# Performance work log

Measured on AMD Instinct MI355X. Metric: run time of the kernel, lower is better.

Reference implementation:

```python
import jax, jax.numpy as jnp
import numpy as np

B, N, M, D, H = 4, 2048, 2048, 1024, 16
HD = D // H


def setup_inputs() -> dict:
    key = jax.random.key(0)
    ks = jax.random.split(key, 16)
    s = 1.0 / np.sqrt(D)
    inp = {
        "Q": jax.random.normal(ks[0], (B, N, D), jnp.float32),
        "K": jax.random.normal(ks[1], (B, M, D), jnp.float32),
        "V": jax.random.normal(ks[2], (B, M, D), jnp.float32),
        "attn_bias": jax.random.normal(ks[3], (B, N, M), jnp.float32),
        "mask": jax.random.randint(ks[4], (B, M), 0, 2).astype(bool),
        # linear params (torch nn.Linear: y = x @ W.T + b)
        "Wq": jax.random.uniform(ks[5], (D, D), jnp.float32, -s, s),
        "bq": jax.random.uniform(ks[6], (D,), jnp.float32, -s, s),
        "Wk": jax.random.uniform(ks[7], (D, D), jnp.float32, -s, s),
        "bk": jax.random.uniform(ks[8], (D,), jnp.float32, -s, s),
        "Wv": jax.random.uniform(ks[9], (D, D), jnp.float32, -s, s),
        "bv": jax.random.uniform(ks[10], (D,), jnp.float32, -s, s),
        "Wo": jax.random.uniform(ks[11], (D, D), jnp.float32, -s, s),
        "bo": jax.random.uniform(ks[12], (D,), jnp.float32, -s, s),
    }
    return inp


def reference(Q, K, V, attn_bias, mask, Wq, bq, Wk, bk, Wv, bv, Wo, bo):
    b, n, d = Q.shape
    m = K.shape[1]
    # bias (B,N,M) -> (B,1,N,M); mask (B,M) True = masked out (-inf)
    bias = attn_bias[:, None, :, :]
    bias = jnp.where(mask[:, None, None, :], -jnp.inf, bias)
    # projections, split heads: (B, H, len, head_dim)
    q = (Q @ Wq.T + bq).reshape(b, n, H, HD).transpose(0, 2, 1, 3)
    k = (K @ Wk.T + bk).reshape(b, m, H, HD).transpose(0, 2, 1, 3)
    v = (V @ Wv.T + bv).reshape(b, m, H, HD).transpose(0, 2, 1, 3)
    scale = 1.0 / np.sqrt(HD).astype(np.float32)
    attn = jnp.einsum("bhid,bhjd->bhij", q * scale, k) + bias
    attn = jax.nn.softmax(attn, axis=-1)
    out = jnp.einsum("bhij,bhjd->bhid", attn, v)
    out = out.transpose(0, 2, 1, 3).reshape(b, n, d)
    return out @ Wo.T + bo
```

## Files before the change

kernel.cpp:

```cpp
#include <hip/hip_runtime.h>
#include <hip/hip_bf16.h>

#define Bq 4
#define Nq 2048
#define Mq 2048
#define Dq 1024
#define Hq 16

typedef __attribute__((ext_vector_type(8))) short short8;
typedef __attribute__((ext_vector_type(4))) short short4v;
typedef __attribute__((ext_vector_type(4))) float floatx4;
typedef __attribute__((ext_vector_type(16))) float floatx16;
typedef __attribute__((ext_vector_type(4))) unsigned uint4v;

static __device__ __forceinline__ short f2bf(float f) {
    __hip_bfloat16 h = __float2bfloat16(f);
    short r;
    __builtin_memcpy(&r, &h, 2);
    return r;
}
static __device__ __forceinline__ float bf2f(short s) {
    unsigned u = ((unsigned)(unsigned short)s) << 16;
    float f;
    __builtin_memcpy(&f, &u, 4);
    return f;
}
static __device__ __forceinline__ unsigned cvtpk_bf16(float lo, float hi) {
    unsigned r;
    asm("v_cvt_pk_bf16_f32 %0, %1, %2" : "=v"(r) : "v"(lo), "v"(hi));
    return r;
}
static __device__ __forceinline__ void swap32(unsigned &a, unsigned &b) {
    asm("v_permlane32_swap_b32 %0, %1" : "+v"(a), "+v"(b));
}
static __device__ __forceinline__ float exp2_fast(float x) {
    float r;
    asm("v_exp_f32 %0, %1" : "=v"(r) : "v"(x));
    return r;
}
static __device__ __forceinline__ void gld16(const void* g, void* l) {
    __builtin_amdgcn_global_load_lds(
        (const __attribute__((address_space(1))) unsigned int*)g,
        (__attribute__((address_space(3))) unsigned int*)l, 16, 0, 0);
}

__global__ void bias_prep(const float* __restrict__ bias, const int* __restrict__ mask,
                          short* __restrict__ out)
{
    const long i = ((long)blockIdx.x * 256 + threadIdx.x) * 8;
    const int m = (int)(i & (Mq - 1));
    const int b = (int)(i >> 22);
    floatx4 f0 = *(const floatx4*)(bias + i);
    floatx4 f1 = *(const floatx4*)(bias + i + 4);
    const int* mp = mask + b * Mq + m;
    short8 o;
#pragma unroll
    for (int e = 0; e < 4; ++e) {
        o[e]     = mp[e]     ? f2bf(-1e38f) : f2bf(f0[e] * 1.44269504f);
        o[e + 4] = mp[e + 4] ? f2bf(-1e38f) : f2bf(f1[e] * 1.44269504f);
    }
    *(short8*)(out + i) = o;
}

__global__ void cvt_bf(const float* __restrict__ s0, const float* __restrict__ s1,
                       const float* __restrict__ s2, const float* __restrict__ s3,
                       short* __restrict__ out, long per)
{
    const int z = blockIdx.y;
    const float* s = (z == 0) ? s0 : (z == 1) ? s1 : (z == 2) ? s2 : s3;
    short* d = out + (long)z * per;
    const long i = ((long)blockIdx.x * 256 + threadIdx.x) * 8;
    floatx4 f0 = *(const floatx4*)(s + i);
    floatx4 f1 = *(const floatx4*)(s + i + 4);
    short8 o;
#pragma unroll
    for (int e = 0; e < 4; ++e) { o[e] = f2bf(f0[e]); o[e + 4] = f2bf(f1[e]); }
    *(short8*)(d + i) = o;
}

struct GB {
    const short* A[3];
    const short* W[3];
    const float* bias[3];
    void* C[3];
    float scale[3];
    int omode[3];
};

__global__ __launch_bounds__(256, 3)
void gemm_all(GB gb, int K)
{
    __shared__ __align__(16) short As[2][128 * 32];
    __shared__ __align__(16) short Bs[2][128 * 32];

    const int z = blockIdx.z;
    const short* Ap = gb.A[z];
    const short* Wp = gb.W[z];

    const int tid = threadIdx.x;
    const int lane = tid & 63;
    const int wid = tid >> 6;
    const int wr = wid >> 1, wc = wid & 1;
    const int g = lane >> 4, c = lane & 15;
    const long row0 = (long)blockIdx.x * 128;
    const int col0 = blockIdx.y * 128;

    const int R0 = tid >> 2;
    const int ub = (tid & 3) ^ ((R0 >> 1) & 3);
    const short* asrc = Ap + (row0 + R0) * (long)K + ub * 8;
    const short* bsrc = Wp + ((long)col0 + R0) * K + ub * 8;

    floatx4 acc[4][4];
#pragma unroll
    for (int i = 0; i < 4; ++i)
#pragma unroll
        for (int j = 0; j < 4; ++j) acc[i][j] = (floatx4)0.0f;

#define GSTAGE(buf, koff) do {                                                \
        char* ad = (char*)As + (buf) * 8192 + wid * 1024;                     \
        char* bd = (char*)Bs + (buf) * 8192 + wid * 1024;                     \
        gld16(asrc + (koff), ad);                                             \
        gld16(asrc + 64L * K + (koff), ad + 4096);                            \
        gld16(bsrc + (koff), bd);                                             \
        gld16(bsrc + 64L * K + (koff), bd + 4096);                            \
    } while (0)

    GSTAGE(0, 0);
    __syncthreads();

    int buf = 0;
    for (int kt = 0; kt < K; kt += 32) {
        if (kt + 32 < K) GSTAGE(buf ^ 1, kt + 32);
        short8* As8 = (short8*)((char*)As + buf * 8192);
        short8* Bs8 = (short8*)((char*)Bs + buf * 8192);
        short8 af[4], bfq[4];
#pragma unroll
        for (int fm = 0; fm < 4; ++fm) {
            const int r = wr * 64 + fm * 16 + c;
            af[fm] = As8[r * 4 + (g ^ ((r >> 1) & 3))];
        }
#pragma unroll
        for (int fn = 0; fn < 4; ++fn) {
            const int cc = wc * 64 + fn * 16 + c;
            bfq[fn] = Bs8[cc * 4 + (g ^ ((cc >> 1) & 3))];
        }
#pragma unroll
        for (int fm = 0; fm < 4; ++fm)
#pragma unroll
            for (int fn = 0; fn < 4; ++fn)
                acc[fm][fn] = __builtin_amdgcn_mfma_f32_16x16x32_bf16(af[fm], bfq[fn], acc[fm][fn], 0, 0, 0);
        __syncthreads();
        buf ^= 1;
    }
#undef GSTAGE

    const float sc = gb.scale[z];
    const float* bp = gb.bias[z];
    const int om = gb.omode[z];
    void* Cp = gb.C[z];
#pragma unroll
    for (int fn = 0; fn < 4; ++fn) {
        const int ccol = col0 + wc * 64 + fn * 16 + c;
        const float bv = bp[ccol];
#pragma unroll
        for (int fm = 0; fm < 4; ++fm) {
            const long r0 = row0 + wr * 64 + fm * 16 + g * 4;
#pragma unroll
            for (int reg = 0; reg < 4; ++reg) {
                const float val = (acc[fm][fn][reg] + bv) * sc;
                const long rr = r0 + reg;
                if (om == 0) {
                    ((short*)Cp)[rr * Dq + ccol] = f2bf(val);
                } else if (om == 1) {
                    const long idx = ((long)(rr >> 11) * Dq + ccol) * (long)Mq + (rr & (Mq - 1));
                    ((short*)Cp)[idx] = f2bf(val);
                } else {
                    ((float*)Cp)[rr * Dq + ccol] = val;
                }
            }
        }
    }
}

__global__ __launch_bounds__(256, 4)
void attn_fused(const short* __restrict__ qg_, const short* __restrict__ kg_,
                const short* __restrict__ vtg, const short* __restrict__ bmg,
                short* __restrict__ outg)
{
    __shared__ __align__(16) short k_lds[2][64 * 64];
    __shared__ __align__(16) short v_lds[2][64 * 64];

    const int tid = threadIdx.x;
    const int lane = tid & 63;
    const int w = tid >> 6;
    const int hi = lane >> 5;
    const int q31 = lane & 31;

    const int blk = blockIdx.x;
    const int bh = blk & 63;
    const int qt = blk >> 6;
    const int b = bh >> 4, h = bh & 15;

    const long qbase = (long)b * Nq + qt * 128 + w * 32;

    short8 qf[4];
#pragma unroll
    for (int ks = 0; ks < 4; ++ks)
        qf[ks] = *(const short8*)(qg_ + (qbase + q31) * Dq + h * 64 + ks * 16 + hi * 8);

    floatx16 oa0 = (floatx16)0.0f, oa1 = (floatx16)0.0f;
    float m_s = -1e37f, l_s = 0.0f;

    const int sr = tid >> 3;
    const int su = (tid & 7) ^ (sr & 7);
    const char* ksrc = (const char*)(kg_ + ((long)b * Mq + sr) * Dq + h * 64 + su * 8);
    const char* vsrc = (const char*)(vtg + ((long)b * Dq + h * 64 + sr) * Mq + su * 8);
    const short* bbase = bmg + (qbase + q31) * Mq + hi * 4;

#define STAGE(bf, kt2) do {                                                   \
        const long j0b = (long)(kt2) * 64;                                    \
        char* kd = (char*)k_lds + (bf) * 8192 + w * 1024;                     \
        char* vd = (char*)v_lds + (bf) * 8192 + w * 1024;                     \
        gld16(ksrc + j0b * (Dq * 2), kd);                                     \
        gld16(ksrc + (j0b + 32) * (Dq * 2), kd + 4096);                       \
        gld16(vsrc + j0b * 2, vd);                                            \
        gld16(vsrc + 32L * Mq * 2 + j0b * 2, vd + 4096);                      \
    } while (0)

#define LOADBB(bb, kt2) do {                                                  \
        const short* brow_ = bbase + (long)(kt2) * 64;                        \
        _Pragma("unroll")                                                     \
        for (int kg = 0; kg < 2; ++kg)                                        \
            _Pragma("unroll")                                                 \
            for (int Qh = 0; Qh < 4; ++Qh)                                    \
                bb[kg * 4 + Qh] = *(const short4v*)(brow_ + kg * 32 + Qh * 8);\
    } while (0)

    short4v bbA[8], bbB[8];

    STAGE(0, 0);
    LOADBB(bbA, 0);
    __syncthreads();

    int buf = 0;
    for (int kt = 0; kt < 32; ++kt) {
        if (kt < 31) STAGE(buf ^ 1, kt + 1);
        LOADBB(bbB, (kt < 31) ? kt + 1 : 31);

        const char* kb = (const char*)k_lds + buf * 8192;
        const char* vb = (const char*)v_lds + buf * 8192;

        floatx16 sa0, sa1;
#pragma unroll
        for (int Qh = 0; Qh < 4; ++Qh)
#pragma unroll
            for (int e = 0; e < 4; ++e) {
                sa0[Qh * 4 + e] = bf2f(bbA[Qh][e]);
                sa1[Qh * 4 + e] = bf2f(bbA[4 + Qh][e]);
            }
        {
            short8 kf[4];
#pragma unroll
            for (int ks = 0; ks < 4; ++ks)
                kf[ks] = *(const short8*)(kb + q31 * 128 + (((2 * ks + hi) ^ (q31 & 7)) * 16));
#pragma unroll
            for (int ks = 0; ks < 4; ++ks)
                sa0 = __builtin_amdgcn_mfma_f32_32x32x16_bf16(kf[ks], qf[ks], sa0, 0, 0, 0);
        }
        {
            short8 kf[4];
            const int r1 = 32 + q31;
#pragma unroll
            for (int ks = 0; ks < 4; ++ks)
                kf[ks] = *(const short8*)(kb + r1 * 128 + (((2 * ks + hi) ^ (r1 & 7)) * 16));
#pragma unroll
            for (int ks = 0; ks < 4; ++ks)
                sa1 = __builtin_amdgcn_mfma_f32_32x32x16_bf16(kf[ks], qf[ks], sa1, 0, 0, 0);
        }

        {
            float a0 = fmaxf(fmaxf(sa0[0], sa0[1]), fmaxf(sa0[2], sa0[3]));
            float a1 = fmaxf(fmaxf(sa0[4], sa0[5]), fmaxf(sa0[6], sa0[7]));
            float a2 = fmaxf(fmaxf(sa0[8], sa0[9]), fmaxf(sa0[10], sa0[11]));
            float a3 = fmaxf(fmaxf(sa0[12], sa0[13]), fmaxf(sa0[14], sa0[15]));
            float a4 = fmaxf(fmaxf(sa1[0], sa1[1]), fmaxf(sa1[2], sa1[3]));
            float a5 = fmaxf(fmaxf(sa1[4], sa1[5]), fmaxf(sa1[6], sa1[7]));
            float a6 = fmaxf(fmaxf(sa1[8], sa1[9]), fmaxf(sa1[10], sa1[11]));
            float a7 = fmaxf(fmaxf(sa1[12], sa1[13]), fmaxf(sa1[14], sa1[15]));
            float pm = fmaxf(fmaxf(fmaxf(a0, a1), fmaxf(a2, a3)),
                             fmaxf(fmaxf(a4, a5), fmaxf(a6, a7)));
            pm = fmaxf(pm, __shfl_xor(pm, 32));
            if (!__all(pm <= m_s + 11.5f)) {
                const float mn = fmaxf(m_s, pm);
                const float al = exp2_fast(m_s - mn);
                l_s *= al;
                oa0 *= al; oa1 *= al;
                m_s = mn;
            }
        }
#pragma unroll
        for (int j = 0; j < 16; ++j) {
            sa0[j] = exp2_fast(sa0[j] - m_s);
            sa1[j] = exp2_fast(sa1[j] - m_s);
        }
        {
            const float t0 = (sa0[0] + sa0[1]) + (sa0[2] + sa0[3]);
            const float t1 = (sa0[4] + sa0[5]) + (sa0[6] + sa0[7]);
            const float t2 = (sa0[8] + sa0[9]) + (sa0[10] + sa0[11]);
            const float t3 = (sa0[12] + sa0[13]) + (sa0[14] + sa0[15]);
            const float t4 = (sa1[0] + sa1[1]) + (sa1[2] + sa1[3]);
            const float t5 = (sa1[4] + sa1[5]) + (sa1[6] + sa1[7]);
            const float t6 = (sa1[8] + sa1[9]) + (sa1[10] + sa1[11]);
            const float t7 = (sa1[12] + sa1[13]) + (sa1[14] + sa1[15]);
            float rs = ((t0 + t1) + (t2 + t3)) + ((t4 + t5) + (t6 + t7));
            rs += __shfl_xor(rs, 32);
            l_s += rs;
        }

        uint4v pw0, pw1, pw2, pw3;
        {
            unsigned w0 = cvtpk_bf16(sa0[0], sa0[1]);
            unsigned w1 = cvtpk_bf16(sa0[2], sa0[3]);
            unsigned w2 = cvtpk_bf16(sa0[4], sa0[5]);
            unsigned w3 = cvtpk_bf16(sa0[6], sa0[7]);
            swap32(w0, w2); swap32(w1, w3);
            pw0[0] = w0; pw0[1] = w1; pw0[2] = w2; pw0[3] = w3;
            unsigned w4 = cvtpk_bf16(sa0[8], sa0[9]);
            unsigned w5 = cvtpk_bf16(sa0[10], sa0[11]);
            unsigned w6 = cvtpk_bf16(sa0[12], sa0[13]);
            unsigned w7 = cvtpk_bf16(sa0[14], sa0[15]);
            swap32(w4, w6); swap32(w5, w7);
            pw1[0] = w4; pw1[1] = w5; pw1[2] = w6; pw1[3] = w7;
            unsigned x0 = cvtpk_bf16(sa1[0], sa1[1]);
            unsigned x1 = cvtpk_bf16(sa1[2], sa1[3]);
            unsigned x2 = cvtpk_bf16(sa1[4], sa1[5]);
            unsigned x3 = cvtpk_bf16(sa1[6], sa1[7]);
            swap32(x0, x2); swap32(x1, x3);
            pw2[0] = x0; pw2[1] = x1; pw2[2] = x2; pw2[3] = x3;
            unsigned x4 = cvtpk_bf16(sa1[8], sa1[9]);
            unsigned x5 = cvtpk_bf16(sa1[10], sa1[11]);
            unsigned x6 = cvtpk_bf16(sa1[12], sa1[13]);
            unsigned x7 = cvtpk_bf16(sa1[14], sa1[15]);
            swap32(x4, x6); swap32(x5, x7);
            pw3[0] = x4; pw3[1] = x5; pw3[2] = x6; pw3[3] = x7;
        }

        {
            short8 vf[4];
#pragma unroll
            for (int ks = 0; ks < 4; ++ks)
                vf[ks] = *(const short8*)(vb + q31 * 128 + (((2 * ks + hi) ^ (q31 & 7)) * 16));
            oa0 = __builtin_amdgcn_mfma_f32_32x32x16_bf16(vf[0], __builtin_bit_cast(short8, pw0), oa0, 0, 0, 0);
            oa0 = __builtin_amdgcn_mfma_f32_32x32x16_bf16(vf[1], __builtin_bit_cast(short8, pw1), oa0, 0, 0, 0);
            oa0 = __builtin_amdgcn_mfma_f32_32x32x16_bf16(vf[2], __builtin_bit_cast(short8, pw2), oa0, 0, 0, 0);
            oa0 = __builtin_amdgcn_mfma_f32_32x32x16_bf16(vf[3], __builtin_bit_cast(short8, pw3), oa0, 0, 0, 0);
        }
        {
            short8 vf[4];
            const int r1 = 32 + q31;
#pragma unroll
            for (int ks = 0; ks < 4; ++ks)
                vf[ks] = *(const short8*)(vb + r1 * 128 + (((2 * ks + hi) ^ (r1 & 7)) * 16));
            oa1 = __builtin_amdgcn_mfma_f32_32x32x16_bf16(vf[0], __builtin_bit_cast(short8, pw0), oa1, 0, 0, 0);
            oa1 = __builtin_amdgcn_mfma_f32_32x32x16_bf16(vf[1], __builtin_bit_cast(short8, pw1), oa1, 0, 0, 0);
            oa1 = __builtin_amdgcn_mfma_f32_32x32x16_bf16(vf[2], __builtin_bit_cast(short8, pw2), oa1, 0, 0, 0);
            oa1 = __builtin_amdgcn_mfma_f32_32x32x16_bf16(vf[3], __builtin_bit_cast(short8, pw3), oa1, 0, 0, 0);
        }

#pragma unroll
        for (int i = 0; i < 8; ++i) bbA[i] = bbB[i];

        __syncthreads();
        buf ^= 1;
    }
#undef STAGE
#undef LOADBB

    const float invl = 1.0f / l_s;
    short* op = outg + (qbase + q31) * Dq + h * 64;
#pragma unroll
    for (int Qh = 0; Qh < 4; ++Qh) {
        short4v t0v, t1v;
#pragma unroll
        for (int e = 0; e < 4; ++e) {
            t0v[e] = f2bf(oa0[Qh * 4 + e] * invl);
            t1v[e] = f2bf(oa1[Qh * 4 + e] * invl);
        }
        *(short4v*)(op + Qh * 8 + hi * 4) = t0v;
        *(short4v*)(op + 32 + Qh * 8 + hi * 4) = t1v;
    }
}

extern "C" void kernel_launch(void* const* d_in, const int* in_sizes, int n_in,
                              void* d_out, int out_size, void* d_ws, size_t ws_size,
                              hipStream_t stream)
{
    const float* Q    = (const float*)d_in[0];
    const float* K    = (const float*)d_in[1];
    const float* V    = (const float*)d_in[2];
    const float* bias = (const float*)d_in[3];
    const int*   mask = (const int*)d_in[4];
    const float* Wq   = (const float*)d_in[5];
    const float* bq   = (const float*)d_in[6];
    const float* Wk   = (const float*)d_in[7];
    const float* bk   = (const float*)d_in[8];
    const float* Wv   = (const float*)d_in[9];
    const float* bv   = (const float*)d_in[10];
    const float* Wo   = (const float*)d_in[11];
    const float* bo   = (const float*)d_in[12];

    const size_t TSZ = (size_t)Bq * Nq * Dq;
    short* q_ws  = (short*)d_ws;
    short* k_ws  = q_ws  + TSZ;
    short* vt_ws = k_ws  + TSZ;
    short* a_ws  = vt_ws + TSZ;
    short* bm_ws = a_ws  + TSZ;
    short* w_ws  = bm_ws + 2 * TSZ;
    short* qin_ws = a_ws;
    short* kin_ws = bm_ws;
    short* vin_ws = bm_ws + TSZ;
    (void)ws_size;

    cvt_bf<<<dim3(512, 4), dim3(256), 0, stream>>>(Wq, Wk, Wv, Wo, w_ws, (long)Dq * Dq);
    cvt_bf<<<dim3(4096, 3), dim3(256), 0, stream>>>(Q, K, V, V, qin_ws, (long)TSZ);

    GB g1{};
    g1.A[0] = qin_ws; g1.A[1] = kin_ws; g1.A[2] = vin_ws;
    g1.W[0] = w_ws; g1.W[1] = w_ws + Dq * Dq; g1.W[2] = w_ws + 2 * Dq * Dq;
    g1.bias[0] = bq; g1.bias[1] = bk; g1.bias[2] = bv;
    g1.C[0] = q_ws; g1.C[1] = k_ws; g1.C[2] = vt_ws;
    g1.scale[0] = 0.125f * 1.44269504f; g1.scale[1] = 1.0f; g1.scale[2] = 1.0f;
    g1.omode[0] = 0; g1.omode[1] = 0; g1.omode[2] = 1;
    gemm_all<<<dim3(64, 8, 3), dim3(256), 0, stream>>>(g1, Dq);

    bias_prep<<<dim3(8192), dim3(256), 0, stream>>>(bias, mask, bm_ws);

    attn_fused<<<dim3(1024), dim3(256), 0, stream>>>(q_ws, k_ws, vt_ws, bm_ws, a_ws);

    GB g2{};
    g2.A[0] = a_ws;
    g2.W[0] = w_ws + 3 * Dq * Dq;
    g2.bias[0] = bo;
    g2.C[0] = d_out;
    g2.scale[0] = 1.0f;
    g2.omode[0] = 2;
    gemm_all<<<dim3(64, 8, 1), dim3(256), 0, stream>>>(g2, Dq);
}
```

Measured before the change: 330.0 us.

## Split attention key range in halves with separate merge kernel

```diff
diff --git a/kernel.cpp b/kernel.cpp
--- a/kernel.cpp
+++ b/kernel.cpp
@@ -9,6 +9,7 @@
 
 typedef __attribute__((ext_vector_type(8))) short short8;
 typedef __attribute__((ext_vector_type(4))) short short4v;
+typedef __attribute__((ext_vector_type(2))) float floatx2;
 typedef __attribute__((ext_vector_type(4))) float floatx4;
 typedef __attribute__((ext_vector_type(16))) float floatx16;
 typedef __attribute__((ext_vector_type(4))) unsigned uint4v;
@@ -182,13 +183,13 @@
     }
 }
 
-__global__ __launch_bounds__(256, 4)
+__global__ __launch_bounds__(256, 8)
 void attn_fused(const short* __restrict__ qg_, const short* __restrict__ kg_,
                 const short* __restrict__ vtg, const short* __restrict__ bmg,
-                short* __restrict__ outg)
-{
-    __shared__ __align__(16) short k_lds[2][64 * 64];
-    __shared__ __align__(16) short v_lds[2][64 * 64];
+                short* __restrict__ pog, float* __restrict__ mlg)
+{
+    __shared__ __align__(16) short k_lds[2][32 * 64];
+    __shared__ __align__(16) short v_lds[2][64 * 32];
 
     const int tid = threadIdx.x;
     const int lane = tid & 63;
@@ -198,8 +199,10 @@
 
     const int blk = blockIdx.x;
     const int bh = blk & 63;
-    const int qt = blk >> 6;
+    const int half = (blk >> 6) & 1;
+    const int qt = blk >> 7;
     const int b = bh >> 4, h = bh & 15;
+    const int m0g = half * 1024;
 
     const long qbase = (long)b * Nq + qt * 128 + w * 32;
 
@@ -213,30 +216,26 @@
 
     const int sr = tid >> 3;
     const int su = (tid & 7) ^ (sr & 7);
-    const char* ksrc = (const char*)(kg_ + ((long)b * Mq + sr) * Dq + h * 64 + su * 8);
-    const char* vsrc = (const char*)(vtg + ((long)b * Dq + h * 64 + sr) * Mq + su * 8);
-    const short* bbase = bmg + (qbase + q31) * Mq + hi * 4;
+    const int vr = tid >> 2;
+    const int vu = (tid & 3) ^ (vr & 3);
+    const char* ksrc = (const char*)(kg_ + ((long)b * Mq + m0g + sr) * Dq + h * 64 + su * 8);
+    const char* vsrc = (const char*)(vtg + ((long)b * Dq + h * 64 + vr) * Mq + m0g + vu * 8);
+    const short* bbase = bmg + (qbase + q31) * Mq + m0g + hi * 4;
 
 #define STAGE(bf, kt2) do {                                                   \
-        const long j0b = (long)(kt2) * 64;                                    \
-        char* kd = (char*)k_lds + (bf) * 8192 + w * 1024;                     \
-        char* vd = (char*)v_lds + (bf) * 8192 + w * 1024;                     \
-        gld16(ksrc + j0b * (Dq * 2), kd);                                     \
-        gld16(ksrc + (j0b + 32) * (Dq * 2), kd + 4096);                       \
-        gld16(vsrc + j0b * 2, vd);                                            \
-        gld16(vsrc + 32L * Mq * 2 + j0b * 2, vd + 4096);                      \
+        const long j0b = (long)(kt2) * 32;                                    \
+        gld16(ksrc + j0b * (Dq * 2), (char*)k_lds + (bf) * 4096 + w * 1024);  \
+        gld16(vsrc + j0b * 2,        (char*)v_lds + (bf) * 4096 + w * 1024);  \
     } while (0)
 
 #define LOADBB(bb, kt2) do {                                                  \
-        const short* brow_ = bbase + (long)(kt2) * 64;                        \
+        const short* brow_ = bbase + (long)(kt2) * 32;                        \
         _Pragma("unroll")                                                     \
-        for (int kg = 0; kg < 2; ++kg)                                        \
-            _Pragma("unroll")                                                 \
-            for (int Qh = 0; Qh < 4; ++Qh)                                    \
-                bb[kg * 4 + Qh] = *(const short4v*)(brow_ + kg * 32 + Qh * 8);\
+        for (int Qh = 0; Qh < 4; ++Qh)                                        \
+            bb[Qh] = *(const short4v*)(brow_ + Qh * 8);                       \
     } while (0)
 
-    short4v bbA[8], bbB[8];
+    short4v bbA[4], bbB[4];
 
     STAGE(0, 0);
     LOADBB(bbA, 0);
@@ -247,17 +246,15 @@
         if (kt < 31) STAGE(buf ^ 1, kt + 1);
         LOADBB(bbB, (kt < 31) ? kt + 1 : 31);
 
-        const char* kb = (const char*)k_lds + buf * 8192;
-        const char* vb = (const char*)v_lds + buf * 8192;
-
-        floatx16 sa0, sa1;
+        const char* kb = (const char*)k_lds + buf * 4096;
+        const char* vb = (const char*)v_lds + buf * 4096;
+
+        floatx16 sa;
 #pragma unroll
         for (int Qh = 0; Qh < 4; ++Qh)
 #pragma unroll
-            for (int e = 0; e < 4; ++e) {
-                sa0[Qh * 4 + e] = bf2f(bbA[Qh][e]);
-                sa1[Qh * 4 + e] = bf2f(bbA[4 + Qh][e]);
-            }
+            for (int e = 0; e < 4; ++e)
+                sa[Qh * 4 + e] = bf2f(bbA[Qh][e]);
         {
             short8 kf[4];
 #pragma unroll
@@ -265,30 +262,15 @@
                 kf[ks] = *(const short8*)(kb + q31 * 128 + (((2 * ks + hi) ^ (q31 & 7)) * 16));
 #pragma unroll
             for (int ks = 0; ks < 4; ++ks)
-                sa0 = __builtin_amdgcn_mfma_f32_32x32x16_bf16(kf[ks], qf[ks], sa0, 0, 0, 0);
-        }
-        {
-            short8 kf[4];
-            const int r1 = 32 + q31;
-#pragma unroll
-            for (int ks = 0; ks < 4; ++ks)
-                kf[ks] = *(const short8*)(kb + r1 * 128 + (((2 * ks + hi) ^ (r1 & 7)) * 16));
-#pragma unroll
-            for (int ks = 0; ks < 4; ++ks)
-                sa1 = __builtin_amdgcn_mfma_f32_32x32x16_bf16(kf[ks], qf[ks], sa1, 0, 0, 0);
-        }
-
-        {
-            float a0 = fmaxf(fmaxf(sa0[0], sa0[1]), fmaxf(sa0[2], sa0[3]));
-            float a1 = fmaxf(fmaxf(sa0[4], sa0[5]), fmaxf(sa0[6], sa0[7]));
-            float a2 = fmaxf(fmaxf(sa0[8], sa0[9]), fmaxf(sa0[10], sa0[11]));
-            float a3 = fmaxf(fmaxf(sa0[12], sa0[13]), fmaxf(sa0[14], sa0[15]));
-            float a4 = fmaxf(fmaxf(sa1[0], sa1[1]), fmaxf(sa1[2], sa1[3]));
-            float a5 = fmaxf(fmaxf(sa1[4], sa1[5]), fmaxf(sa1[6], sa1[7]));
-            float a6 = fmaxf(fmaxf(sa1[8], sa1[9]), fmaxf(sa1[10], sa1[11]));
-            float a7 = fmaxf(fmaxf(sa1[12], sa1[13]), fmaxf(sa1[14], sa1[15]));
-            float pm = fmaxf(fmaxf(fmaxf(a0, a1), fmaxf(a2, a3)),
-                             fmaxf(fmaxf(a4, a5), fmaxf(a6, a7)));
+                sa = __builtin_amdgcn_mfma_f32_32x32x16_bf16(kf[ks], qf[ks], sa, 0, 0, 0);
+        }
+
+        {
+            float a0 = fmaxf(fmaxf(sa[0], sa[1]), fmaxf(sa[2], sa[3]));
+            float a1 = fmaxf(fmaxf(sa[4], sa[5]), fmaxf(sa[6], sa[7]));
+            float a2 = fmaxf(fmaxf(sa[8], sa[9]), fmaxf(sa[10], sa[11]));
+            float a3 = fmaxf(fmaxf(sa[12], sa[13]), fmaxf(sa[14], sa[15]));
+            float pm = fmaxf(fmaxf(a0, a1), fmaxf(a2, a3));
             pm = fmaxf(pm, __shfl_xor(pm, 32));
             if (!__all(pm <= m_s + 11.5f)) {
                 const float mn = fmaxf(m_s, pm);
@@ -299,76 +281,54 @@
             }
         }
 #pragma unroll
-        for (int j = 0; j < 16; ++j) {
-            sa0[j] = exp2_fast(sa0[j] - m_s);
-            sa1[j] = exp2_fast(sa1[j] - m_s);
-        }
-        {
-            const float t0 = (sa0[0] + sa0[1]) + (sa0[2] + sa0[3]);
-            const float t1 = (sa0[4] + sa0[5]) + (sa0[6] + sa0[7]);
-            const float t2 = (sa0[8] + sa0[9]) + (sa0[10] + sa0[11]);
-            const float t3 = (sa0[12] + sa0[13]) + (sa0[14] + sa0[15]);
-            const float t4 = (sa1[0] + sa1[1]) + (sa1[2] + sa1[3]);
-            const float t5 = (sa1[4] + sa1[5]) + (sa1[6] + sa1[7]);
-            const float t6 = (sa1[8] + sa1[9]) + (sa1[10] + sa1[11]);
-            const float t7 = (sa1[12] + sa1[13]) + (sa1[14] + sa1[15]);
-            float rs = ((t0 + t1) + (t2 + t3)) + ((t4 + t5) + (t6 + t7));
+        for (int j = 0; j < 16; ++j)
+            sa[j] = exp2_fast(sa[j] - m_s);
+        {
+            const float t0 = (sa[0] + sa[1]) + (sa[2] + sa[3]);
+            const float t1 = (sa[4] + sa[5]) + (sa[6] + sa[7]);
+            const float t2 = (sa[8] + sa[9]) + (sa[10] + sa[11]);
+            const float t3 = (sa[12] + sa[13]) + (sa[14] + sa[15]);
+            float rs = (t0 + t1) + (t2 + t3);
             rs += __shfl_xor(rs, 32);
             l_s += rs;
         }
 
-        uint4v pw0, pw1, pw2, pw3;
-        {
-            unsigned w0 = cvtpk_bf16(sa0[0], sa0[1]);
-            unsigned w1 = cvtpk_bf16(sa0[2], sa0[3]);
-            unsigned w2 = cvtpk_bf16(sa0[4], sa0[5]);
-            unsigned w3 = cvtpk_bf16(sa0[6], sa0[7]);
+        uint4v pw0, pw1;
+        {
+            unsigned w0 = cvtpk_bf16(sa[0], sa[1]);
+            unsigned w1 = cvtpk_bf16(sa[2], sa[3]);
+            unsigned w2 = cvtpk_bf16(sa[4], sa[5]);
+            unsigned w3 = cvtpk_bf16(sa[6], sa[7]);
             swap32(w0, w2); swap32(w1, w3);
             pw0[0] = w0; pw0[1] = w1; pw0[2] = w2; pw0[3] = w3;
-            unsigned w4 = cvtpk_bf16(sa0[8], sa0[9]);
-            unsigned w5 = cvtpk_bf16(sa0[10], sa0[11]);
-            unsigned w6 = cvtpk_bf16(sa0[12], sa0[13]);
-            unsigned w7 = cvtpk_bf16(sa0[14], sa0[15]);
+            unsigned w4 = cvtpk_bf16(sa[8], sa[9]);
+            unsigned w5 = cvtpk_bf16(sa[10], sa[11]);
+            unsigned w6 = cvtpk_bf16(sa[12], sa[13]);
+            unsigned w7 = cvtpk_bf16(sa[14], sa[15]);
             swap32(w4, w6); swap32(w5, w7);
             pw1[0] = w4; pw1[1] = w5; pw1[2] = w6; pw1[3] = w7;
-            unsigned x0 = cvtpk_bf16(sa1[0], sa1[1]);
-            unsigned x1 = cvtpk_bf16(sa1[2], sa1[3]);
-            unsigned x2 = cvtpk_bf16(sa1[4], sa1[5]);
-            unsigned x3 = cvtpk_bf16(sa1[6], sa1[7]);
-            swap32(x0, x2); swap32(x1, x3);
-            pw2[0] = x0; pw2[1] = x1; pw2[2] = x2; pw2[3] = x3;
-            unsigned x4 = cvtpk_bf16(sa1[8], sa1[9]);
-            unsigned x5 = cvtpk_bf16(sa1[10], sa1[11]);
-            unsigned x6 = cvtpk_bf16(sa1[12], sa1[13]);
-            unsigned x7 = cvtpk_bf16(sa1[14], sa1[15]);
-            swap32(x4, x6); swap32(x5, x7);
-            pw3[0] = x4; pw3[1] = x5; pw3[2] = x6; pw3[3] = x7;
-        }
-
-        {
-            short8 vf[4];
-#pragma unroll
-            for (int ks = 0; ks < 4; ++ks)
-                vf[ks] = *(const short8*)(vb + q31 * 128 + (((2 * ks + hi) ^ (q31 & 7)) * 16));
+        }
+
+        {
+            short8 vf[2];
+#pragma unroll
+            for (int ks = 0; ks < 2; ++ks)
+                vf[ks] = *(const short8*)(vb + q31 * 64 + (((2 * ks + hi) ^ (q31 & 3)) * 16));
             oa0 = __builtin_amdgcn_mfma_f32_32x32x16_bf16(vf[0], __builtin_bit_cast(short8, pw0), oa0, 0, 0, 0);
             oa0 = __builtin_amdgcn_mfma_f32_32x32x16_bf16(vf[1], __builtin_bit_cast(short8, pw1), oa0, 0, 0, 0);
-            oa0 = __builtin_amdgcn_mfma_f32_32x32x16_bf16(vf[2], __builtin_bit_cast(short8, pw2), oa0, 0, 0, 0);
-            oa0 = __builtin_amdgcn_mfma_f32_32x32x16_bf16(vf[3], __builtin_bit_cast(short8, pw3), oa0, 0, 0, 0);
-        }
-        {
-            short8 vf[4];
+        }
+        {
+            short8 vf[2];
             const int r1 = 32 + q31;
 #pragma unroll
-            for (int ks = 0; ks < 4; ++ks)
-                vf[ks] = *(const short8*)(vb + r1 * 128 + (((2 * ks + hi) ^ (r1 & 7)) * 16));
+            for (int ks = 0; ks < 2; ++ks)
+                vf[ks] = *(const short8*)(vb + r1 * 64 + (((2 * ks + hi) ^ (r1 & 3)) * 16));
             oa1 = __builtin_amdgcn_mfma_f32_32x32x16_bf16(vf[0], __builtin_bit_cast(short8, pw0), oa1, 0, 0, 0);
             oa1 = __builtin_amdgcn_mfma_f32_32x32x16_bf16(vf[1], __builtin_bit_cast(short8, pw1), oa1, 0, 0, 0);
-            oa1 = __builtin_amdgcn_mfma_f32_32x32x16_bf16(vf[2], __builtin_bit_cast(short8, pw2), oa1, 0, 0, 0);
-            oa1 = __builtin_amdgcn_mfma_f32_32x32x16_bf16(vf[3], __builtin_bit_cast(short8, pw3), oa1, 0, 0, 0);
-        }
-
-#pragma unroll
-        for (int i = 0; i < 8; ++i) bbA[i] = bbB[i];
+        }
+
+#pragma unroll
+        for (int i = 0; i < 4; ++i) bbA[i] = bbB[i];
 
         __syncthreads();
         buf ^= 1;
@@ -376,18 +336,55 @@
 #undef STAGE
 #undef LOADBB
 
-    const float invl = 1.0f / l_s;
-    short* op = outg + (qbase + q31) * Dq + h * 64;
+    short* op = pog + (size_t)half * ((size_t)Bq * Nq * Dq) + (qbase + q31) * Dq + h * 64;
 #pragma unroll
     for (int Qh = 0; Qh < 4; ++Qh) {
         short4v t0v, t1v;
 #pragma unroll
         for (int e = 0; e < 4; ++e) {
-            t0v[e] = f2bf(oa0[Qh * 4 + e] * invl);
-            t1v[e] = f2bf(oa1[Qh * 4 + e] * invl);
+            t0v[e] = f2bf(oa0[Qh * 4 + e]);
+            t1v[e] = f2bf(oa1[Qh * 4 + e]);
         }
         *(short4v*)(op + Qh * 8 + hi * 4) = t0v;
         *(short4v*)(op + 32 + Qh * 8 + hi * 4) = t1v;
+    }
+    if (!hi) {
+        const int mi = (b * Hq + h) * Nq + qt * 128 + w * 32 + q31;
+        floatx2 v; v[0] = m_s; v[1] = l_s;
+        *(floatx2*)(mlg + 2 * ((size_t)half * (Bq * Hq * Nq) + mi)) = v;
+    }
+}
+
+__global__ void merge_halves(const short* __restrict__ pog, const float* __restrict__ mlg,
+                             short* __restrict__ outg)
+{
+    const int R = blockIdx.x * 256 + threadIdx.x;
+    const int b = R >> 15;
+    const int h = (R >> 11) & 15;
+    const int n = R & (Nq - 1);
+    const int mi = (b * Hq + h) * Nq + n;
+    const floatx2 v0 = *(const floatx2*)(mlg + 2 * mi);
+    const floatx2 v1 = *(const floatx2*)(mlg + 2 * (Bq * Hq * Nq + mi));
+    const float m = fmaxf(v0[0], v1[0]);
+    const float a0 = exp2_fast(v0[0] - m);
+    const float a1 = exp2_fast(v1[0] - m);
+    const float inv = 1.0f / (v0[1] * a0 + v1[1] * a1);
+    const float s0 = a0 * inv, s1 = a1 * inv;
+
+    const size_t base = ((size_t)(b * Nq + n)) * Dq + h * 64;
+    const size_t TSZ = (size_t)Bq * Nq * Dq;
+    const short* p0 = pog + base;
+    const short* p1 = pog + TSZ + base;
+    short* op = outg + base;
+#pragma unroll
+    for (int oct = 0; oct < 8; ++oct) {
+        short8 x0 = *(const short8*)(p0 + oct * 8);
+        short8 x1 = *(const short8*)(p1 + oct * 8);
+        short8 o;
+#pragma unroll
+        for (int e = 0; e < 8; ++e)
+            o[e] = f2bf(bf2f(x0[e]) * s0 + bf2f(x1[e]) * s1);
+        *(short8*)(op + oct * 8) = o;
     }
 }
 
@@ -416,6 +413,8 @@
     short* a_ws  = vt_ws + TSZ;
     short* bm_ws = a_ws  + TSZ;
     short* w_ws  = bm_ws + 2 * TSZ;
+    short* po_ws = w_ws  + (size_t)4 * Dq * Dq;
+    float* ml_ws = (float*)(po_ws + 2 * TSZ);
     short* qin_ws = a_ws;
     short* kin_ws = bm_ws;
     short* vin_ws = bm_ws + TSZ;
@@ -435,7 +434,8 @@
 
     bias_prep<<<dim3(8192), dim3(256), 0, stream>>>(bias, mask, bm_ws);
 
-    attn_fused<<<dim3(1024), dim3(256), 0, stream>>>(q_ws, k_ws, vt_ws, bm_ws, a_ws);
+    attn_fused<<<dim3(2048), dim3(256), 0, stream>>>(q_ws, k_ws, vt_ws, bm_ws, po_ws, ml_ws);
+    merge_halves<<<dim3(512), dim3(256), 0, stream>>>(po_ws, ml_ws, a_ws);
 
     GB g2{};
     g2.A[0] = a_ws;
```

Result: slower. 778.8 us (+136.0%).

## Software-pipeline QK^T one tile ahead with triple-buffered K in LDS

Applied to the files above, without the earlier changes.

```diff
diff --git a/kernel.cpp b/kernel.cpp
--- a/kernel.cpp
+++ b/kernel.cpp
@@ -187,7 +187,7 @@
                 const short* __restrict__ vtg, const short* __restrict__ bmg,
                 short* __restrict__ outg)
 {
-    __shared__ __align__(16) short k_lds[2][64 * 64];
+    __shared__ __align__(16) short k_lds[3][64 * 64];
     __shared__ __align__(16) short v_lds[2][64 * 64];
 
     const int tid = threadIdx.x;
@@ -217,76 +217,77 @@
     const char* vsrc = (const char*)(vtg + ((long)b * Dq + h * 64 + sr) * Mq + su * 8);
     const short* bbase = bmg + (qbase + q31) * Mq + hi * 4;
 
-#define STAGE(bf, kt2) do {                                                   \
+#define STAGE_K(slot, kt2) do {                                               \
         const long j0b = (long)(kt2) * 64;                                    \
-        char* kd = (char*)k_lds + (bf) * 8192 + w * 1024;                     \
-        char* vd = (char*)v_lds + (bf) * 8192 + w * 1024;                     \
+        char* kd = (char*)k_lds + (slot) * 8192 + w * 1024;                   \
         gld16(ksrc + j0b * (Dq * 2), kd);                                     \
         gld16(ksrc + (j0b + 32) * (Dq * 2), kd + 4096);                       \
+    } while (0)
+
+#define STAGE_V(slot, kt2) do {                                               \
+        const long j0b = (long)(kt2) * 64;                                    \
+        char* vd = (char*)v_lds + (slot) * 8192 + w * 1024;                   \
         gld16(vsrc + j0b * 2, vd);                                            \
         gld16(vsrc + 32L * Mq * 2 + j0b * 2, vd + 4096);                      \
     } while (0)
 
-#define LOADBB(bb, kt2) do {                                                  \
+#define QKT(sa0_, sa1_, kslot, kt2) do {                                      \
         const short* brow_ = bbase + (long)(kt2) * 64;                        \
         _Pragma("unroll")                                                     \
-        for (int kg = 0; kg < 2; ++kg)                                        \
+        for (int Qh = 0; Qh < 4; ++Qh) {                                      \
+            const short4v b4a = *(const short4v*)(brow_ + Qh * 8);            \
+            const short4v b4b = *(const short4v*)(brow_ + 32 + Qh * 8);       \
             _Pragma("unroll")                                                 \
-            for (int Qh = 0; Qh < 4; ++Qh)                                    \
-                bb[kg * 4 + Qh] = *(const short4v*)(brow_ + kg * 32 + Qh * 8);\
+            for (int e = 0; e < 4; ++e) {                                     \
+                sa0_[Qh * 4 + e] = bf2f(b4a[e]);                              \
+                sa1_[Qh * 4 + e] = bf2f(b4b[e]);                              \
+            }                                                                 \
+        }                                                                     \
+        const char* kb_ = (const char*)k_lds + (kslot) * 8192;                \
+        {                                                                     \
+            short8 kf[4];                                                     \
+            _Pragma("unroll")                                                 \
+            for (int ks = 0; ks < 4; ++ks)                                    \
+                kf[ks] = *(const short8*)(kb_ + q31 * 128 + (((2 * ks + hi) ^ (q31 & 7)) * 16)); \
+            _Pragma("unroll")                                                 \
+            for (int ks = 0; ks < 4; ++ks)                                    \
+                sa0_ = __builtin_amdgcn_mfma_f32_32x32x16_bf16(kf[ks], qf[ks], sa0_, 0, 0, 0); \
+        }                                                                     \
+        {                                                                     \
+            short8 kf[4];                                                     \
+            const int r1_ = 32 + q31;                                         \
+            _Pragma("unroll")                                                 \
+            for (int ks = 0; ks < 4; ++ks)                                    \
+                kf[ks] = *(const short8*)(kb_ + r1_ * 128 + (((2 * ks + hi) ^ (r1_ & 7)) * 16)); \
+            _Pragma("unroll")                                                 \
+            for (int ks = 0; ks < 4; ++ks)                                    \
+                sa1_ = __builtin_amdgcn_mfma_f32_32x32x16_bf16(kf[ks], qf[ks], sa1_, 0, 0, 0); \
+        }                                                                     \
     } while (0)
 
-    short4v bbA[8], bbB[8];
-
-    STAGE(0, 0);
-    LOADBB(bbA, 0);
+    floatx16 saA0, saA1, saB0, saB1;
+
+    STAGE_K(0, 0);
+    STAGE_V(0, 0);
     __syncthreads();
-
-    int buf = 0;
-    for (int kt = 0; kt < 32; ++kt) {
-        if (kt < 31) STAGE(buf ^ 1, kt + 1);
-        LOADBB(bbB, (kt < 31) ? kt + 1 : 31);
-
-        const char* kb = (const char*)k_lds + buf * 8192;
-        const char* vb = (const char*)v_lds + buf * 8192;
-
-        floatx16 sa0, sa1;
-#pragma unroll
-        for (int Qh = 0; Qh < 4; ++Qh)
-#pragma unroll
-            for (int e = 0; e < 4; ++e) {
-                sa0[Qh * 4 + e] = bf2f(bbA[Qh][e]);
-                sa1[Qh * 4 + e] = bf2f(bbA[4 + Qh][e]);
-            }
+    QKT(saA0, saA1, 0, 0);
+    STAGE_K(1, 1);
+    __syncthreads();
+
+    for (int t = 0; t < 32; ++t) {
+        if (t < 31) STAGE_V((t + 1) & 1, t + 1);
+        if (t < 30) STAGE_K((t + 2) % 3, t + 2);
+        if (t < 31) QKT(saB0, saB1, (t + 1) % 3, t + 1);
+
         {
-            short8 kf[4];
-#pragma unroll
-            for (int ks = 0; ks < 4; ++ks)
-                kf[ks] = *(const short8*)(kb + q31 * 128 + (((2 * ks + hi) ^ (q31 & 7)) * 16));
-#pragma unroll
-            for (int ks = 0; ks < 4; ++ks)
-                sa0 = __builtin_amdgcn_mfma_f32_32x32x16_bf16(kf[ks], qf[ks], sa0, 0, 0, 0);
-        }
-        {
-            short8 kf[4];
-            const int r1 = 32 + q31;
-#pragma unroll
-            for (int ks = 0; ks < 4; ++ks)
-                kf[ks] = *(const short8*)(kb + r1 * 128 + (((2 * ks + hi) ^ (r1 & 7)) * 16));
-#pragma unroll
-            for (int ks = 0; ks < 4; ++ks)
-                sa1 = __builtin_amdgcn_mfma_f32_32x32x16_bf16(kf[ks], qf[ks], sa1, 0, 0, 0);
-        }
-
-        {
-            float a0 = fmaxf(fmaxf(sa0[0], sa0[1]), fmaxf(sa0[2], sa0[3]));
-            float a1 = fmaxf(fmaxf(sa0[4], sa0[5]), fmaxf(sa0[6], sa0[7]));
-            float a2 = fmaxf(fmaxf(sa0[8], sa0[9]), fmaxf(sa0[10], sa0[11]));
-            float a3 = fmaxf(fmaxf(sa0[12], sa0[13]), fmaxf(sa0[14], sa0[15]));
-            float a4 = fmaxf(fmaxf(sa1[0], sa1[1]), fmaxf(sa1[2], sa1[3]));
-            float a5 = fmaxf(fmaxf(sa1[4], sa1[5]), fmaxf(sa1[6], sa1[7]));
-            float a6 = fmaxf(fmaxf(sa1[8], sa1[9]), fmaxf(sa1[10], sa1[11]));
-            float a7 = fmaxf(fmaxf(sa1[12], sa1[13]), fmaxf(sa1[14], sa1[15]));
+            float a0 = fmaxf(fmaxf(saA0[0], saA0[1]), fmaxf(saA0[2], saA0[3]));
+            float a1 = fmaxf(fmaxf(saA0[4], saA0[5]), fmaxf(saA0[6], saA0[7]));
+            float a2 = fmaxf(fmaxf(saA0[8], saA0[9]), fmaxf(saA0[10], saA0[11]));
+            float a3 = fmaxf(fmaxf(saA0[12], saA0[13]), fmaxf(saA0[14], saA0[15]));
+            float a4 = fmaxf(fmaxf(saA1[0], saA1[1]), fmaxf(saA1[2], saA1[3]));
+            float a5 = fmaxf(fmaxf(saA1[4], saA1[5]), fmaxf(saA1[6], saA1[7]));
+            float a6 = fmaxf(fmaxf(saA1[8], saA1[9]), fmaxf(saA1[10], saA1[11]));
+            float a7 = fmaxf(fmaxf(saA1[12], saA1[13]), fmaxf(saA1[14], saA1[15]));
             float pm = fmaxf(fmaxf(fmaxf(a0, a1), fmaxf(a2, a3)),
                              fmaxf(fmaxf(a4, a5), fmaxf(a6, a7)));
             pm = fmaxf(pm, __shfl_xor(pm, 32));
@@ -300,18 +301,18 @@
         }
 #pragma unroll
         for (int j = 0; j < 16; ++j) {
-            sa0[j] = exp2_fast(sa0[j] - m_s);
-            sa1[j] = exp2_fast(sa1[j] - m_s);
+            saA0[j] = exp2_fast(saA0[j] - m_s);
+            saA1[j] = exp2_fast(saA1[j] - m_s);
         }
         {
-            const float t0 = (sa0[0] + sa0[1]) + (sa0[2] + sa0[3]);
-            const float t1 = (sa0[4] + sa0[5]) + (sa0[6] + sa0[7]);
-            const float t2 = (sa0[8] + sa0[9]) + (sa0[10] + sa0[11]);
-            const float t3 = (sa0[12] + sa0[13]) + (sa0[14] + sa0[15]);
-            const float t4 = (sa1[0] + sa1[1]) + (sa1[2] + sa1[3]);
-            const float t5 = (sa1[4] + sa1[5]) + (sa1[6] + sa1[7]);
-            const float t6 = (sa1[8] + sa1[9]) + (sa1[10] + sa1[11]);
-            const float t7 = (sa1[12] + sa1[13]) + (sa1[14] + sa1[15]);
+            const float t0 = (saA0[0] + saA0[1]) + (saA0[2] + saA0[3]);
+            const float t1 = (saA0[4] + saA0[5]) + (saA0[6] + saA0[7]);
+            const float t2 = (saA0[8] + saA0[9]) + (saA0[10] + saA0[11]);
+            const float t3 = (saA0[12] + saA0[13]) + (saA0[14] + saA0[15]);
+            const float t4 = (saA1[0] + saA1[1]) + (saA1[2] + saA1[3]);
+            const float t5 = (saA1[4] + saA1[5]) + (saA1[6] + saA1[7]);
+            const float t6 = (saA1[8] + saA1[9]) + (saA1[10] + saA1[11]);
+            const float t7 = (saA1[12] + saA1[13]) + (saA1[14] + saA1[15]);
             float rs = ((t0 + t1) + (t2 + t3)) + ((t4 + t5) + (t6 + t7));
             rs += __shfl_xor(rs, 32);
             l_s += rs;
@@ -319,32 +320,33 @@
 
         uint4v pw0, pw1, pw2, pw3;
         {
-            unsigned w0 = cvtpk_bf16(sa0[0], sa0[1]);
-            unsigned w1 = cvtpk_bf16(sa0[2], sa0[3]);
-            unsigned w2 = cvtpk_bf16(sa0[4], sa0[5]);
-            unsigned w3 = cvtpk_bf16(sa0[6], sa0[7]);
+            unsigned w0 = cvtpk_bf16(saA0[0], saA0[1]);
+            unsigned w1 = cvtpk_bf16(saA0[2], saA0[3]);
+            unsigned w2 = cvtpk_bf16(saA0[4], saA0[5]);
+            unsigned w3 = cvtpk_bf16(saA0[6], saA0[7]);
             swap32(w0, w2); swap32(w1, w3);
             pw0[0] = w0; pw0[1] = w1; pw0[2] = w2; pw0[3] = w3;
-            unsigned w4 = cvtpk_bf16(sa0[8], sa0[9]);
-            unsigned w5 = cvtpk_bf16(sa0[10], sa0[11]);
-            unsigned w6 = cvtpk_bf16(sa0[12], sa0[13]);
-            unsigned w7 = cvtpk_bf16(sa0[14], sa0[15]);
+            unsigned w4 = cvtpk_bf16(saA0[8], saA0[9]);
+            unsigned w5 = cvtpk_bf16(saA0[10], saA0[11]);
+            unsigned w6 = cvtpk_bf16(saA0[12], saA0[13]);
+            unsigned w7 = cvtpk_bf16(saA0[14], saA0[15]);
             swap32(w4, w6); swap32(w5, w7);
             pw1[0] = w4; pw1[1] = w5; pw1[2] = w6; pw1[3] = w7;
-            unsigned x0 = cvtpk_bf16(sa1[0], sa1[1]);
-            unsigned x1 = cvtpk_bf16(sa1[2], sa1[3]);
-            unsigned x2 = cvtpk_bf16(sa1[4], sa1[5]);
-            unsigned x3 = cvtpk_bf16(sa1[6], sa1[7]);
+            unsigned x0 = cvtpk_bf16(saA1[0], saA1[1]);
+            unsigned x1 = cvtpk_bf16(saA1[2], saA1[3]);
+            unsigned x2 = cvtpk_bf16(saA1[4], saA1[5]);
+            unsigned x3 = cvtpk_bf16(saA1[6], saA1[7]);
             swap32(x0, x2); swap32(x1, x3);
             pw2[0] = x0; pw2[1] = x1; pw2[2] = x2; pw2[3] = x3;
-            unsigned x4 = cvtpk_bf16(sa1[8], sa1[9]);
-            unsigned x5 = cvtpk_bf16(sa1[10], sa1[11]);
-            unsigned x6 = cvtpk_bf16(sa1[12], sa1[13]);
-            unsigned x7 = cvtpk_bf16(sa1[14], sa1[15]);
+            unsigned x4 = cvtpk_bf16(saA1[8], saA1[9]);
+            unsigned x5 = cvtpk_bf16(saA1[10], saA1[11]);
+            unsigned x6 = cvtpk_bf16(saA1[12], saA1[13]);
+            unsigned x7 = cvtpk_bf16(saA1[14], saA1[15]);
             swap32(x4, x6); swap32(x5, x7);
             pw3[0] = x4; pw3[1] = x5; pw3[2] = x6; pw3[3] = x7;
         }
 
+        const char* vb = (const char*)v_lds + (t & 1) * 8192;
         {
             short8 vf[4];
 #pragma unroll
@@ -367,14 +369,13 @@
             oa1 = __builtin_amdgcn_mfma_f32_32x32x16_bf16(vf[3], __builtin_bit_cast(short8, pw3), oa1, 0, 0, 0);
         }
 
-#pragma unroll
-        for (int i = 0; i < 8; ++i) bbA[i] = bbB[i];
-
         __syncthreads();
-        buf ^= 1;
+        saA0 = saB0;
+        saA1 = saB1;
     }
-#undef STAGE
-#undef LOADBB
+#undef STAGE_K
+#undef STAGE_V
+#undef QKT
 
     const float invl = 1.0f / l_s;
     short* op = outg + (qbase + q31) * Dq + h * 64;
```

After: 417.4 us. +26.5%, slower.
